# Kernel optimization log

Measured on AMD Instinct MI355X. Metric: run time of the kernel, lower is better.

## Reference

```python
import jax, jax.numpy as jnp
import numpy as np

FRAC_BITS = 16            # fixed-point fractional bits (MPC fixedpoint precision)
SCALE = float(1 << FRAC_BITS)

def fxp(v):
    """Emulate dup_with_precision: round value to the fixed-point grid with
    FRAC_BITS fractional bits. Straight-through (identity) gradient, matching
    the MPC backward pass which propagates gradients through truncation."""
    return v + jax.lax.stop_gradient(jnp.round(v * SCALE) / SCALE - v)


def setup_inputs() -> dict:
    key = jax.random.key(0)
    kx, kw = jax.random.split(key)
    in_dim, out_dim, batch = 4096, 4096, 2048
    x = jax.random.normal(kx, (batch, in_dim), dtype=jnp.float32)
    # Dense_Local init: w ~ N(0, 1/sqrt(in_dim+1)), b = zeros
    w = jax.random.normal(kw, (in_dim, out_dim), dtype=jnp.float32) / np.sqrt(in_dim + 1)
    b = jnp.zeros((out_dim,), dtype=jnp.float32)
    return {"x": x, "w": w, "b": b}


def reference(x, w, b):
    # quantize operands to the fixed-point grid (values live on the grid in MPC)
    xq = fxp(x)
    wq = fxp(w)
    # y = x @ w, then dup_with_precision(x.fixedpoint): truncate product back
    y = fxp(jnp.matmul(xq, wq))           # [batch, out_dim]
    # + bias
    y = y + fxp(b)
    # secure ReLU: s = drelu_local(y) (sign bit), y = relu(y, s) = y * s
    s = y >= 0
    y = jnp.where(s, y, jnp.zeros((), dtype=y.dtype))
    # final dup_with_precision(new_fixedpoint=x.fixedpoint)
    return fxp(y)
```

## Files before the change

### kernel.cpp

```cpp
#include <hip/hip_runtime.h>
#include <hip/hip_bf16.h>
#include <stdint.h>

#define M_DIM 2048
#define N_DIM 4096
#define K_DIM 4096

#define NT 64

typedef short short8 __attribute__((ext_vector_type(8)));
typedef float f32x4 __attribute__((ext_vector_type(4)));

typedef __attribute__((address_space(1))) unsigned int gu32;
typedef __attribute__((address_space(3))) unsigned int lu32;

__device__ static inline unsigned short f32_to_bf16(float f) {
  union { float f; unsigned int u; } v; v.f = f;
  unsigned int u = v.u;
  u += 0x7FFFu + ((u >> 16) & 1u);
  return (unsigned short)(u >> 16);
}

__global__ void prep_kernel(const float* __restrict__ x, unsigned short* __restrict__ xa,
                            const float* __restrict__ wsrc, unsigned short* __restrict__ wt) {
  __shared__ unsigned short tile[64][64 + 8];
  int bid = blockIdx.x;
  int t = threadIdx.x;
  if (bid < 4096) {
    size_t i = ((size_t)bid * 256 + t) * 8;
    f32x4 a = *(const f32x4*)(x + i);
    f32x4 b = *(const f32x4*)(x + i + 4);
    short8 o;
    o[0] = (short)f32_to_bf16(a[0]); o[1] = (short)f32_to_bf16(a[1]);
    o[2] = (short)f32_to_bf16(a[2]); o[3] = (short)f32_to_bf16(a[3]);
    o[4] = (short)f32_to_bf16(b[0]); o[5] = (short)f32_to_bf16(b[1]);
    o[6] = (short)f32_to_bf16(b[2]); o[7] = (short)f32_to_bf16(b[3]);
    *(short8*)(xa + i) = o;
    return;
  }
  int b2 = bid - 4096;
  int bn = (b2 & 63) * 64;
  int bk = (b2 >> 6) * 64;
  int c4 = (t & 15) * 4;
  int r0 = t >> 4;
#pragma unroll
  for (int p = 0; p < 4; ++p) {
    int r = r0 + p * 16;
    f32x4 v = *(const f32x4*)(wsrc + (size_t)(bk + r) * N_DIM + bn + c4);
    tile[c4 + 0][r] = f32_to_bf16(v[0]);
    tile[c4 + 1][r] = f32_to_bf16(v[1]);
    tile[c4 + 2][r] = f32_to_bf16(v[2]);
    tile[c4 + 3][r] = f32_to_bf16(v[3]);
  }
  __syncthreads();
  int orow = t >> 2;
  int oc = (t & 3) * 16;
  short8 lo, hi;
#pragma unroll
  for (int j = 0; j < 8; ++j) {
    lo[j] = (short)tile[orow][oc + j];
    hi[j] = (short)tile[orow][oc + 8 + j];
  }
  unsigned short* op = wt + (size_t)(bn + orow) * K_DIM + bk + oc;
  *(short8*)(op) = lo;
  *(short8*)(op + 8) = hi;
}


__global__ __launch_bounds__(512) void gemm8_kernel(
    const unsigned short* __restrict__ A, const unsigned short* __restrict__ Bt,
    const float* __restrict__ bias, float* __restrict__ C) {
  __shared__ unsigned short smA[3 * 24576];
  char* smemc = (char*)&smA[0];

  const int tid = threadIdx.x;
  const int lane = tid & 63;
  const int w = tid >> 6;
  const int wm = w >> 2, wn = w & 3;

  const int id = blockIdx.x;
  const int x = id & 7, j = id >> 3;
  const int by = ((x >> 2) << 3) + (j >> 2);
  const int bx = ((x & 3) << 2) + (j & 3);
  const int r0 = by * 128, c0 = bx * 256;

  const int l8 = lane >> 3, l7 = lane & 7;
  const int chunkE = ((l7 ^ l8) << 3);
  const unsigned short* Ag = A + (size_t)(r0 + w * 16 + l8) * K_DIM + chunkE;
  const unsigned short* Bg = Bt + (size_t)(c0 + w * 32 + l8) * K_DIM + chunkE;
  const int aL0 = w * 2048;
  const int bL0 = 16384 + w * 4096;

#define GL(gp, ldsoff) __builtin_amdgcn_global_load_lds((gu32*)(gp), (lu32*)(smemc + (ldsoff)), 16, 0, 0)
#define STAGE_ALL(t, sb)                                               \
  do {                                                                 \
    GL(Ag + (size_t)(t) * 64, (sb) + aL0);                             \
    GL(Ag + (size_t)(t) * 64 + 8 * (size_t)K_DIM, (sb) + aL0 + 1024);  \
    GL(Bg + (size_t)(t) * 64, (sb) + bL0);                             \
    GL(Bg + (size_t)(t) * 64 + 8 * (size_t)K_DIM, (sb) + bL0 + 1024);  \
    GL(Bg + (size_t)(t) * 64 + 16 * (size_t)K_DIM, (sb) + bL0 + 2048); \
    GL(Bg + (size_t)(t) * 64 + 24 * (size_t)K_DIM, (sb) + bL0 + 3072); \
  } while (0)

  const int l15 = lane & 15, hi = lane >> 4;
  const int aR = (wm * 64 + l15) * 64;
  const int bR = 8192 + (wn * 64 + l15) * 64;
  const int slot0 = ((hi ^ l7) << 3);
  const int slot1 = (((4 + hi) ^ l7) << 3);

  f32x4 acc[4][4] = {};

  STAGE_ALL(0, 0);
  STAGE_ALL(1, 49152);

  int cs = 0;
  for (int t = 0; t < NT; ++t) {
    const int sE = cs * 24576;
    const int stB = (cs == 0 ? 2 : cs - 1) * 49152;
    const bool doStage = (t + 2) < NT;

    if (t < NT - 1) asm volatile("s_waitcnt vmcnt(6) lgkmcnt(0)" ::: "memory");
    else            asm volatile("s_waitcnt vmcnt(0) lgkmcnt(0)" ::: "memory");
    __builtin_amdgcn_sched_barrier(0);
    asm volatile("s_barrier" ::: "memory");

    short8 a0[4], b0[4], a1[4], b1[4];
#pragma unroll
    for (int m = 0; m < 4; ++m) a0[m] = *(const short8*)(smA + sE + aR + m * 1024 + slot0);
#pragma unroll
    for (int n = 0; n < 4; ++n) b0[n] = *(const short8*)(smA + sE + bR + n * 1024 + slot0);
    if (doStage) STAGE_ALL(t + 2, stB);
#pragma unroll
    for (int m = 0; m < 4; ++m) a1[m] = *(const short8*)(smA + sE + aR + m * 1024 + slot1);
#pragma unroll
    for (int n = 0; n < 4; ++n) b1[n] = *(const short8*)(smA + sE + bR + n * 1024 + slot1);

#pragma unroll
    for (int m = 0; m < 4; ++m)
#pragma unroll
      for (int n = 0; n < 4; ++n)
        acc[m][n] = __builtin_amdgcn_mfma_f32_16x16x32_bf16(a0[m], b0[n], acc[m][n], 0, 0, 0);
#pragma unroll
    for (int m = 0; m < 4; ++m)
#pragma unroll
      for (int n = 0; n < 4; ++n)
        acc[m][n] = __builtin_amdgcn_mfma_f32_16x16x32_bf16(a1[m], b1[n], acc[m][n], 0, 0, 0);

    cs = (cs == 2) ? 0 : cs + 1;
  }

  const float S = 65536.0f, IS = 1.0f / 65536.0f;
  const int lr = hi * 4;
#pragma unroll
  for (int n = 0; n < 4; ++n) {
    int gcol = c0 + wn * 64 + n * 16 + l15;
    float bq = rintf(bias[gcol] * S) * IS;
#pragma unroll
    for (int m = 0; m < 4; ++m) {
      int grow = r0 + wm * 64 + m * 16 + lr;
      float* outp = C + (size_t)grow * N_DIM + gcol;
#pragma unroll
      for (int r = 0; r < 4; ++r) {
        float t = rintf(acc[m][n][r] * S) * IS + bq;
        t = t > 0.0f ? t : 0.0f;
        outp[(size_t)r * N_DIM] = t;
      }
    }
  }
#undef GL
#undef STAGE_ALL
}

__global__ __launch_bounds__(256, 2) void gemm_fb_kernel(
    const float* __restrict__ Xf, const float* __restrict__ Wf,
    const float* __restrict__ bias, float* __restrict__ C) {
  __shared__ unsigned short As[128][64];
  __shared__ unsigned short Bs[128][64];
  int tid = threadIdx.x;
  int lane = tid & 63;
  int wid = tid >> 6;
  int wr = wid >> 1, wc = wid & 1;
  int r0 = blockIdx.y * 128;
  int c0 = blockIdx.x * 128;
  f32x4 acc[4][4] = {};
  for (int kt = 0; kt < K_DIM / 64; ++kt) {
    __syncthreads();
    int ar = tid >> 1;
    int ac = (tid & 1) * 32;
    const float* xp = Xf + (size_t)(r0 + ar) * K_DIM + kt * 64 + ac;
#pragma unroll
    for (int jj = 0; jj < 8; ++jj) {
      f32x4 v = *(const f32x4*)(xp + jj * 4);
      As[ar][ac + jj * 4 + 0] = f32_to_bf16(v[0]);
      As[ar][ac + jj * 4 + 1] = f32_to_bf16(v[1]);
      As[ar][ac + jj * 4 + 2] = f32_to_bf16(v[2]);
      As[ar][ac + jj * 4 + 3] = f32_to_bf16(v[3]);
    }
    int bk_ = tid >> 2;
    int bc = (tid & 3) * 32;
    const float* wp = Wf + (size_t)(kt * 64 + bk_) * N_DIM + c0 + bc;
#pragma unroll
    for (int jj = 0; jj < 8; ++jj) {
      f32x4 v = *(const f32x4*)(wp + jj * 4);
      Bs[bc + jj * 4 + 0][bk_] = f32_to_bf16(v[0]);
      Bs[bc + jj * 4 + 1][bk_] = f32_to_bf16(v[1]);
      Bs[bc + jj * 4 + 2][bk_] = f32_to_bf16(v[2]);
      Bs[bc + jj * 4 + 3][bk_] = f32_to_bf16(v[3]);
    }
    __syncthreads();
#pragma unroll
    for (int ks = 0; ks < 2; ++ks) {
      int co = ks * 32 + (lane >> 4) * 8;
      int rA = wr * 64 + (lane & 15);
      int rB = wc * 64 + (lane & 15);
      short8 a[4], b[4];
#pragma unroll
      for (int m = 0; m < 4; ++m) a[m] = *(const short8*)&As[rA + m * 16][co];
#pragma unroll
      for (int n = 0; n < 4; ++n) b[n] = *(const short8*)&Bs[rB + n * 16][co];
#pragma unroll
      for (int m = 0; m < 4; ++m)
#pragma unroll
        for (int n = 0; n < 4; ++n)
          acc[m][n] = __builtin_amdgcn_mfma_f32_16x16x32_bf16(a[m], b[n], acc[m][n], 0, 0, 0);
    }
  }
  const float S = 65536.0f, IS = 1.0f / 65536.0f;
  int lr = (lane >> 4) * 4;
  int lc = lane & 15;
#pragma unroll
  for (int n = 0; n < 4; ++n) {
    int gcol = c0 + wc * 64 + n * 16 + lc;
    float bq = rintf(bias[gcol] * S) * IS;
#pragma unroll
    for (int m = 0; m < 4; ++m) {
      int grow = r0 + wr * 64 + m * 16 + lr;
      float* outp = C + (size_t)grow * N_DIM + gcol;
#pragma unroll
      for (int r = 0; r < 4; ++r) {
        float t = rintf(acc[m][n][r] * S) * IS + bq;
        t = t > 0.0f ? t : 0.0f;
        outp[(size_t)r * N_DIM] = t;
      }
    }
  }
}

extern "C" void kernel_launch(void* const* d_in, const int* in_sizes, int n_in,
                              void* d_out, int out_size, void* d_ws, size_t ws_size,
                              hipStream_t stream) {
  const float* x = (const float*)d_in[0];
  const float* w = (const float*)d_in[1];
  const float* b = (const float*)d_in[2];
  float* out = (float*)d_out;

  size_t needA = (size_t)M_DIM * K_DIM * sizeof(unsigned short);
  size_t needB = (size_t)K_DIM * N_DIM * sizeof(unsigned short);

  if (ws_size >= needA + needB) {
    unsigned short* Abf = (unsigned short*)d_ws;
    unsigned short* Btbf = (unsigned short*)((char*)d_ws + needA);
    prep_kernel<<<8192, 256, 0, stream>>>(x, Abf, w, Btbf);
    gemm8_kernel<<<256, 512, 0, stream>>>(Abf, Btbf, b, out);
  } else {
    gemm_fb_kernel<<<dim3(N_DIM / 128, M_DIM / 128), 256, 0, stream>>>(x, w, b, out);
  }
}
```

Baseline: 86.78 us.

## Fuse activation bf16 conversion into GEMM A-tile staging, drop separate pass

Removes the separate x→bf16 conversion pass from the prep kernel. The GEMM now loads fp32 activations directly into registers, converts them to bf16, and writes them to LDS, overlapping this with the first MFMA half. This saves one full read and write of the activation matrix plus part of the prep launch. In exchange, A-tile global traffic doubles, since each tile is reread as fp32 by every column block, and the staging uses register loads and VGPRs instead of async LDS loads. The vmcnt wait is adjusted to match.

```diff
diff --git a/kernel.cpp b/kernel.cpp
--- a/kernel.cpp
+++ b/kernel.cpp
@@ -21,24 +21,19 @@
   return (unsigned short)(u >> 16);
 }
 
-__global__ void prep_kernel(const float* __restrict__ x, unsigned short* __restrict__ xa,
-                            const float* __restrict__ wsrc, unsigned short* __restrict__ wt) {
+__device__ static inline short8 cvt8(f32x4 a, f32x4 b) {
+  short8 o;
+  o[0] = (short)f32_to_bf16(a[0]); o[1] = (short)f32_to_bf16(a[1]);
+  o[2] = (short)f32_to_bf16(a[2]); o[3] = (short)f32_to_bf16(a[3]);
+  o[4] = (short)f32_to_bf16(b[0]); o[5] = (short)f32_to_bf16(b[1]);
+  o[6] = (short)f32_to_bf16(b[2]); o[7] = (short)f32_to_bf16(b[3]);
+  return o;
+}
+
+__global__ void prep_kernel(const float* __restrict__ wsrc, unsigned short* __restrict__ wt) {
   __shared__ unsigned short tile[64][64 + 8];
-  int bid = blockIdx.x;
+  int b2 = blockIdx.x;
   int t = threadIdx.x;
-  if (bid < 4096) {
-    size_t i = ((size_t)bid * 256 + t) * 8;
-    f32x4 a = *(const f32x4*)(x + i);
-    f32x4 b = *(const f32x4*)(x + i + 4);
-    short8 o;
-    o[0] = (short)f32_to_bf16(a[0]); o[1] = (short)f32_to_bf16(a[1]);
-    o[2] = (short)f32_to_bf16(a[2]); o[3] = (short)f32_to_bf16(a[3]);
-    o[4] = (short)f32_to_bf16(b[0]); o[5] = (short)f32_to_bf16(b[1]);
-    o[6] = (short)f32_to_bf16(b[2]); o[7] = (short)f32_to_bf16(b[3]);
-    *(short8*)(xa + i) = o;
-    return;
-  }
-  int b2 = bid - 4096;
   int bn = (b2 & 63) * 64;
   int bk = (b2 >> 6) * 64;
   int c4 = (t & 15) * 4;
@@ -68,7 +63,7 @@
 
 
 __global__ __launch_bounds__(512) void gemm8_kernel(
-    const unsigned short* __restrict__ A, const unsigned short* __restrict__ Bt,
+    const float* __restrict__ Xf, const unsigned short* __restrict__ Bt,
     const float* __restrict__ bias, float* __restrict__ C) {
   __shared__ unsigned short smA[3 * 24576];
   char* smemc = (char*)&smA[0];
@@ -86,16 +81,14 @@
 
   const int l8 = lane >> 3, l7 = lane & 7;
   const int chunkE = ((l7 ^ l8) << 3);
-  const unsigned short* Ag = A + (size_t)(r0 + w * 16 + l8) * K_DIM + chunkE;
+  const float* Axf = Xf + (size_t)(r0 + w * 16 + l8) * K_DIM + chunkE;
   const unsigned short* Bg = Bt + (size_t)(c0 + w * 32 + l8) * K_DIM + chunkE;
-  const int aL0 = w * 2048;
+  const int aL0 = w * 2048 + lane * 16;
   const int bL0 = 16384 + w * 4096;
 
 #define GL(gp, ldsoff) __builtin_amdgcn_global_load_lds((gu32*)(gp), (lu32*)(smemc + (ldsoff)), 16, 0, 0)
-#define STAGE_ALL(t, sb)                                               \
+#define STAGE_B(t, sb)                                                 \
   do {                                                                 \
-    GL(Ag + (size_t)(t) * 64, (sb) + aL0);                             \
-    GL(Ag + (size_t)(t) * 64 + 8 * (size_t)K_DIM, (sb) + aL0 + 1024);  \
     GL(Bg + (size_t)(t) * 64, (sb) + bL0);                             \
     GL(Bg + (size_t)(t) * 64 + 8 * (size_t)K_DIM, (sb) + bL0 + 1024);  \
     GL(Bg + (size_t)(t) * 64 + 16 * (size_t)K_DIM, (sb) + bL0 + 2048); \
@@ -110,8 +103,22 @@
 
   f32x4 acc[4][4] = {};
 
-  STAGE_ALL(0, 0);
-  STAGE_ALL(1, 49152);
+  {
+    f32x4 v0 = *(const f32x4*)(Axf);
+    f32x4 v1 = *(const f32x4*)(Axf + 4);
+    f32x4 v2 = *(const f32x4*)(Axf + 8 * (size_t)K_DIM);
+    f32x4 v3 = *(const f32x4*)(Axf + 8 * (size_t)K_DIM + 4);
+    *(short8*)(smemc + 0 + aL0) = cvt8(v0, v1);
+    *(short8*)(smemc + 0 + aL0 + 1024) = cvt8(v2, v3);
+    f32x4 u0 = *(const f32x4*)(Axf + 64);
+    f32x4 u1 = *(const f32x4*)(Axf + 64 + 4);
+    f32x4 u2 = *(const f32x4*)(Axf + 64 + 8 * (size_t)K_DIM);
+    f32x4 u3 = *(const f32x4*)(Axf + 64 + 8 * (size_t)K_DIM + 4);
+    *(short8*)(smemc + 49152 + aL0) = cvt8(u0, u1);
+    *(short8*)(smemc + 49152 + aL0 + 1024) = cvt8(u2, u3);
+  }
+  STAGE_B(0, 0);
+  STAGE_B(1, 49152);
 
   int cs = 0;
   for (int t = 0; t < NT; ++t) {
@@ -119,7 +126,7 @@
     const int stB = (cs == 0 ? 2 : cs - 1) * 49152;
     const bool doStage = (t + 2) < NT;
 
-    if (t < NT - 1) asm volatile("s_waitcnt vmcnt(6) lgkmcnt(0)" ::: "memory");
+    if (t < NT - 1) asm volatile("s_waitcnt vmcnt(4) lgkmcnt(0)" ::: "memory");
     else            asm volatile("s_waitcnt vmcnt(0) lgkmcnt(0)" ::: "memory");
     __builtin_amdgcn_sched_barrier(0);
     asm volatile("s_barrier" ::: "memory");
@@ -129,7 +136,16 @@
     for (int m = 0; m < 4; ++m) a0[m] = *(const short8*)(smA + sE + aR + m * 1024 + slot0);
 #pragma unroll
     for (int n = 0; n < 4; ++n) b0[n] = *(const short8*)(smA + sE + bR + n * 1024 + slot0);
-    if (doStage) STAGE_ALL(t + 2, stB);
+
+    f32x4 av0, av1, av2, av3;
+    if (doStage) {
+      av0 = *(const f32x4*)(Axf + (size_t)(t + 2) * 64);
+      av1 = *(const f32x4*)(Axf + (size_t)(t + 2) * 64 + 4);
+      av2 = *(const f32x4*)(Axf + (size_t)(t + 2) * 64 + 8 * (size_t)K_DIM);
+      av3 = *(const f32x4*)(Axf + (size_t)(t + 2) * 64 + 8 * (size_t)K_DIM + 4);
+      STAGE_B(t + 2, stB);
+    }
+
 #pragma unroll
     for (int m = 0; m < 4; ++m) a1[m] = *(const short8*)(smA + sE + aR + m * 1024 + slot1);
 #pragma unroll
@@ -140,6 +156,12 @@
 #pragma unroll
       for (int n = 0; n < 4; ++n)
         acc[m][n] = __builtin_amdgcn_mfma_f32_16x16x32_bf16(a0[m], b0[n], acc[m][n], 0, 0, 0);
+
+    if (doStage) {
+      *(short8*)(smemc + stB + aL0) = cvt8(av0, av1);
+      *(short8*)(smemc + stB + aL0 + 1024) = cvt8(av2, av3);
+    }
+
 #pragma unroll
     for (int m = 0; m < 4; ++m)
 #pragma unroll
@@ -168,7 +190,7 @@
     }
   }
 #undef GL
-#undef STAGE_ALL
+#undef STAGE_B
 }
 
 __global__ __launch_bounds__(256, 2) void gemm_fb_kernel(
@@ -254,14 +276,12 @@
   const float* b = (const float*)d_in[2];
   float* out = (float*)d_out;
 
-  size_t needA = (size_t)M_DIM * K_DIM * sizeof(unsigned short);
   size_t needB = (size_t)K_DIM * N_DIM * sizeof(unsigned short);
 
-  if (ws_size >= needA + needB) {
-    unsigned short* Abf = (unsigned short*)d_ws;
-    unsigned short* Btbf = (unsigned short*)((char*)d_ws + needA);
-    prep_kernel<<<8192, 256, 0, stream>>>(x, Abf, w, Btbf);
-    gemm8_kernel<<<256, 512, 0, stream>>>(Abf, Btbf, b, out);
+  if (ws_size >= needB) {
+    unsigned short* Btbf = (unsigned short*)d_ws;
+    prep_kernel<<<4096, 256, 0, stream>>>(w, Btbf);
+    gemm8_kernel<<<256, 512, 0, stream>>>(x, Btbf, b, out);
   } else {
     gemm_fb_kernel<<<dim3(N_DIM / 128, M_DIM / 128), 256, 0, stream>>>(x, w, b, out);
   }
```

Measured after the change: 96.67 us. 11.4% more time.
